# Performance work log

Hardware: AMD Instinct MI355X
Metric: run time of the kernel (lower is better)

## Reference

```python
import jax, jax.numpy as jnp
import numpy as np


def setup_inputs() -> dict:
    key = jax.random.key(0)
    k1, k2, k3 = jax.random.split(key, 3)
    shape = (2, 16, 2048, 64)  # (b, num_heads, seq_len, d_k)
    Q = jax.random.normal(k1, shape, dtype=jnp.float32)
    K = jax.random.normal(k2, shape, dtype=jnp.float32)
    V = jax.random.normal(k3, shape, dtype=jnp.float32)
    return {"Q": Q, "K": K, "V": V}


def reference(Q, K, V):
    # Mathematically identical to the blockwise online-softmax loop:
    # causal softmax attention with scale 1/sqrt(d_k), plus logsumexp L.
    d_k = Q.shape[-1]
    seq_len = Q.shape[2]
    scale = 1.0 / np.sqrt(d_k).astype(np.float32)
    # scores: [b, h, q, k]
    S = jnp.einsum("bhqd,bhkd->bhqk", Q, K) * scale
    causal_mask = jnp.tril(jnp.ones((seq_len, seq_len), dtype=bool))  # k_pos <= q_pos
    S = jnp.where(causal_mask, S, -jnp.inf)
    # L_i = m_i + log(l_i) == logsumexp over key dim (every row has >=1 valid key)
    L = jax.nn.logsumexp(S, axis=-1, keepdims=True)  # [b, h, q, 1]
    P = jnp.exp(S - L)  # normalized probabilities (deferred-normalization result)
    O = jnp.einsum("bhqk,bhkd->bhqd", P, V)
    return O, L
```

## Files before the change

### kernel.cpp

```cpp
#include <hip/hip_runtime.h>
#include <hip/hip_bf16.h>

#define S_LEN 2048
#define DH    64
#define NBH   32
#define KSCALE 0.1803368801111f
#define LN2    0.6931471805599453f
#define MB2    4.0f

typedef short v4s __attribute__((ext_vector_type(4)));
typedef short v8s __attribute__((ext_vector_type(8)));
typedef float v4f __attribute__((ext_vector_type(4)));

__device__ __forceinline__ unsigned short f2bf(float f){
  union { float f; unsigned int u; } v; v.f = f;
  return (unsigned short)((v.u + 0x7FFFu + ((v.u >> 16) & 1u)) >> 16);
}

__device__ __forceinline__ void gld16(void* lds, const void* g){
  __builtin_amdgcn_global_load_lds(
      (const __attribute__((address_space(1))) unsigned int*)g,
      (__attribute__((address_space(3))) unsigned int*)lds, 16, 0, 0);
}

__global__ __launch_bounds__(256) void prep(const float* __restrict__ K,
                                            const float* __restrict__ V,
                                            unsigned short* __restrict__ Kf,
                                            unsigned short* __restrict__ Vf){
  __shared__ unsigned short s[64 * 72];
  const int t   = blockIdx.x;
  const int bh  = blockIdx.y;
  const int tid = threadIdx.x;

  const float* Ksrc = K + ((size_t)bh * S_LEN + t * 64) * DH;
  #pragma unroll
  for (int i = 0; i < 4; ++i){
    int f = tid + i * 256;
    float4 v = ((const float4*)Ksrc)[f];
    int row = f >> 4, col = (f & 15) * 4;
    ushort4 o; o.x = f2bf(v.x); o.y = f2bf(v.y); o.z = f2bf(v.z); o.w = f2bf(v.w);
    *(ushort4*)(&s[row * 72 + col]) = o;
  }
  __syncthreads();
  unsigned short* KfT = Kf + ((size_t)bh * 32 + t) * 4096;
  #pragma unroll
  for (int i = 0; i < 2; ++i){
    int item = tid + i * 256;
    int c = item >> 6, l = item & 63;
    int kb = c >> 1, h = c & 1;
    v8s frag = *(const v8s*)(&s[(kb * 16 + (l & 15)) * 72 + h * 32 + (l >> 4) * 8]);
    *(v8s*)(&KfT[c * 512 + l * 8]) = frag;
  }
  __syncthreads();

  const float* Vsrc = V + ((size_t)bh * S_LEN + t * 64) * DH;
  #pragma unroll
  for (int i = 0; i < 4; ++i){
    int f = tid + i * 256;
    float4 v = ((const float4*)Vsrc)[f];
    int k = f >> 4, d = (f & 15) * 4;
    s[(d + 0) * 72 + k] = f2bf(v.x);
    s[(d + 1) * 72 + k] = f2bf(v.y);
    s[(d + 2) * 72 + k] = f2bf(v.z);
    s[(d + 3) * 72 + k] = f2bf(v.w);
  }
  __syncthreads();
  unsigned short* VfT = Vf + ((size_t)bh * 32 + t) * 4096;
  #pragma unroll
  for (int i = 0; i < 2; ++i){
    int item = tid + i * 256;
    int c = item >> 6, l = item & 63;
    int kb = c >> 1, dp = c & 1;
    int kk = kb * 16 + (l >> 4) * 4;
    v4s a = *(const v4s*)(&s[((dp * 2 + 0) * 16 + (l & 15)) * 72 + kk]);
    v4s b = *(const v4s*)(&s[((dp * 2 + 1) * 16 + (l & 15)) * 72 + kk]);
    v8s fr; fr[0]=a[0]; fr[1]=a[1]; fr[2]=a[2]; fr[3]=a[3];
            fr[4]=b[0]; fr[5]=b[1]; fr[6]=b[2]; fr[7]=b[3];
    *(v8s*)(&VfT[c * 512 + l * 8]) = fr;
  }
}

__global__ __launch_bounds__(256, 3) void fa_fwd(
    const float* __restrict__ Q,
    const unsigned short* __restrict__ Kf,
    const unsigned short* __restrict__ Vf,
    float* __restrict__ O, float* __restrict__ L)
{
  __shared__ __align__(16) char smem[2][16384];

  const int tid  = threadIdx.x;
  const int w    = tid >> 6;
  const int lane = tid & 63;
  const int lq   = lane & 15;
  const int g    = lane >> 4;
  const int bid  = blockIdx.x;
  const int o    = bid >> 5;
  const int hi   = o >> 3, lo = o & 7;
  const int qt   = hi * 8 + ((hi & 1) ? (7 - lo) : lo);
  const int bh   = bid & 31;
  const int M    = qt + 1;

  const unsigned short* KfB = Kf + (size_t)bh * 32 * 4096;
  const unsigned short* VfB = Vf + (size_t)bh * 32 * 4096;

  auto issue = [&](int t, char* buf){
    #pragma unroll
    for (int i = 0; i < 2; ++i){
      const int slot = tid + i * 256;
      gld16(buf        + slot * 16, KfB + (size_t)t * 4096 + slot * 8);
      gld16(buf + 8192 + slot * 16, VfB + (size_t)t * 4096 + slot * 8);
    }
  };

  v8s qf[4][2];
  #pragma unroll
  for (int s = 0; s < 4; ++s){
    const float* qp = Q + (size_t)(bh * S_LEN + qt * 64 + s * 16 + lq) * DH + g * 8;
    #pragma unroll
    for (int h = 0; h < 2; ++h){
      float4 a = *(const float4*)(qp + h * 32);
      float4 b = *(const float4*)(qp + h * 32 + 4);
      v8s qv;
      qv[0]=(short)f2bf(a.x*KSCALE); qv[1]=(short)f2bf(a.y*KSCALE);
      qv[2]=(short)f2bf(a.z*KSCALE); qv[3]=(short)f2bf(a.w*KSCALE);
      qv[4]=(short)f2bf(b.x*KSCALE); qv[5]=(short)f2bf(b.y*KSCALE);
      qv[6]=(short)f2bf(b.z*KSCALE); qv[7]=(short)f2bf(b.w*KSCALE);
      qf[s][h] = qv;
    }
  }

  issue(0, smem[0]);

  const v4f zero  = {0.f, 0.f, 0.f, 0.f};
  const v4f minit = {-MB2, -MB2, -MB2, -MB2};
  v4f acc[4][4];
  #pragma unroll
  for (int s = 0; s < 4; ++s)
    #pragma unroll
    for (int db = 0; db < 4; ++db) acc[s][db] = zero;
  float l4[4] = {0.f, 0.f, 0.f, 0.f};

  const int kb    = w;
  const int koff0 = (kb * 2    ) * 1024 + lane * 16;
  const int koff1 = (kb * 2 + 1) * 1024 + lane * 16;

  for (int t = 0; t < M; ++t){
    const int tn = (t + 1 < M) ? t + 1 : t;
    issue(tn, smem[(t + 1) & 1]);
    asm volatile("s_waitcnt vmcnt(4)" ::: "memory");
    __builtin_amdgcn_s_barrier();
    __builtin_amdgcn_sched_barrier(0);

    const char* kbase = smem[t & 1];
    const char* vbase = smem[t & 1] + 8192;

    v8s kf0 = *(const v8s*)(kbase + koff0);
    v8s kf1 = *(const v8s*)(kbase + koff1);
    v8s vv0 = *(const v8s*)(vbase + koff0);
    v8s vv1 = *(const v8s*)(vbase + koff1);
    v4s vv[4] = { {vv0[0],vv0[1],vv0[2],vv0[3]}, {vv0[4],vv0[5],vv0[6],vv0[7]},
                  {vv1[0],vv1[1],vv1[2],vv1[3]}, {vv1[4],vv1[5],vv1[6],vv1[7]} };

    float p4[4][4];
    __builtin_amdgcn_s_setprio(1);
    #pragma unroll
    for (int s = 0; s < 4; ++s){
      v4f st = minit;
      st = __builtin_amdgcn_mfma_f32_16x16x32_bf16(kf0, qf[s][0], st, 0, 0, 0);
      st = __builtin_amdgcn_mfma_f32_16x16x32_bf16(kf1, qf[s][1], st, 0, 0, 0);
      p4[s][0] = st[0]; p4[s][1] = st[1]; p4[s][2] = st[2]; p4[s][3] = st[3];
    }
    __builtin_amdgcn_s_setprio(0);

    if (t == qt){
      #pragma unroll
      for (int s = 0; s < 4; ++s)
        #pragma unroll
        for (int r = 0; r < 4; ++r)
          if (kb * 16 + g * 4 + r > s * 16 + lq) p4[s][r] = -INFINITY;
    }

    v4s pf[4];
    #pragma unroll
    for (int s = 0; s < 4; ++s){
      #pragma unroll
      for (int r = 0; r < 4; ++r){
        const float pe = __builtin_amdgcn_exp2f(p4[s][r]);
        p4[s][r] = pe;
        l4[s] += pe;
      }
      unsigned u0, u1;
      asm("v_cvt_pk_bf16_f32 %0, %1, %2" : "=v"(u0) : "v"(p4[s][0]), "v"(p4[s][1]));
      asm("v_cvt_pk_bf16_f32 %0, %1, %2" : "=v"(u1) : "v"(p4[s][2]), "v"(p4[s][3]));
      union { unsigned u[2]; v4s s4; } P; P.u[0] = u0; P.u[1] = u1;
      pf[s] = P.s4;
    }

    __builtin_amdgcn_s_setprio(1);
    #pragma unroll
    for (int s = 0; s < 4; ++s){
      acc[s][0] = __builtin_amdgcn_mfma_f32_16x16x16bf16_1k(vv[0], pf[s], acc[s][0], 0, 0, 0);
      acc[s][1] = __builtin_amdgcn_mfma_f32_16x16x16bf16_1k(vv[1], pf[s], acc[s][1], 0, 0, 0);
      acc[s][2] = __builtin_amdgcn_mfma_f32_16x16x16bf16_1k(vv[2], pf[s], acc[s][2], 0, 0, 0);
      acc[s][3] = __builtin_amdgcn_mfma_f32_16x16x16bf16_1k(vv[3], pf[s], acc[s][3], 0, 0, 0);
    }
    __builtin_amdgcn_s_setprio(0);
    __builtin_amdgcn_s_barrier();
    __builtin_amdgcn_sched_barrier(0);
  }

  asm volatile("s_waitcnt vmcnt(0)" ::: "memory");
  __builtin_amdgcn_sched_barrier(0);
  __syncthreads();

  #pragma unroll
  for (int s = 0; s < 4; ++s){
    l4[s] += __shfl_xor(l4[s], 16);
    l4[s] += __shfl_xor(l4[s], 32);
  }
  float* Lr = (float*)smem[1];
  if (lane < 16){
    #pragma unroll
    for (int s = 0; s < 4; ++s) Lr[(w * 4 + s) * 16 + lane] = l4[s];
  }
  __syncthreads();
  const float lfw = Lr[(0 * 4 + w) * 16 + lq] + Lr[(1 * 4 + w) * 16 + lq]
                  + Lr[(2 * 4 + w) * 16 + lq] + Lr[(3 * 4 + w) * 16 + lq];
  const float invw = 1.f / lfw;

  v4f* Or = (v4f*)smem[0];
  float* Ob = O + ((size_t)bh * S_LEN + qt * 64 + w * 16 + lq) * DH;
  #pragma unroll
  for (int db = 0; db < 4; ++db){
    __syncthreads();
    #pragma unroll
    for (int s = 0; s < 4; ++s) Or[((w * 4 + s) * 16 + lq) * 4 + g] = acc[s][db];
    __syncthreads();
    v4f o2 = Or[((0 * 4 + w) * 16 + lq) * 4 + g] + Or[((1 * 4 + w) * 16 + lq) * 4 + g]
           + Or[((2 * 4 + w) * 16 + lq) * 4 + g] + Or[((3 * 4 + w) * 16 + lq) * 4 + g];
    o2 *= invw;
    *(v4f*)(Ob + db * 16 + g * 4) = o2;
  }
  if (lane < 16)
    L[(size_t)bh * S_LEN + qt * 64 + w * 16 + lane] = logf(lfw) + MB2 * LN2;
}

__global__ __launch_bounds__(64) void fa_naive(
    const float* __restrict__ Q, const float* __restrict__ K,
    const float* __restrict__ V, float* __restrict__ O, float* __restrict__ L)
{
  const int q  = blockIdx.x;
  const int bh = blockIdx.y;
  const int d  = threadIdx.x;
  const float qv = Q[(size_t)(bh * S_LEN + q) * DH + d];
  float m = -INFINITY, l = 0.f, o = 0.f;
  for (int k = 0; k <= q; ++k){
    float s = qv * K[(size_t)(bh * S_LEN + k) * DH + d];
    #pragma unroll
    for (int off = 32; off > 0; off >>= 1) s += __shfl_xor(s, off);
    s *= 0.125f;
    const float mn = fmaxf(m, s);
    const float sfc = expf(m - mn);
    const float pe = expf(s - mn);
    l = l * sfc + pe;
    o = o * sfc + pe * V[(size_t)(bh * S_LEN + k) * DH + d];
    m = mn;
  }
  O[(size_t)(bh * S_LEN + q) * DH + d] = o / l;
  if (d == 0) L[(size_t)bh * S_LEN + q] = m + logf(l);
}

extern "C" void kernel_launch(void* const* d_in, const int* in_sizes, int n_in,
                              void* d_out, int out_size, void* d_ws, size_t ws_size,
                              hipStream_t stream)
{
  (void)in_sizes; (void)n_in; (void)out_size;
  const float* Q = (const float*)d_in[0];
  const float* K = (const float*)d_in[1];
  const float* V = (const float*)d_in[2];
  float* O = (float*)d_out;
  float* L = O + (size_t)NBH * S_LEN * DH;

  const size_t half = (size_t)NBH * S_LEN * DH * sizeof(unsigned short);
  if (ws_size >= 2 * half){
    unsigned short* Kf = (unsigned short*)d_ws;
    unsigned short* Vf = Kf + (size_t)NBH * S_LEN * DH;
    prep<<<dim3(S_LEN / 64, NBH), 256, 0, stream>>>(K, V, Kf, Vf);
    fa_fwd<<<dim3(1024), 256, 0, stream>>>(Q, Kf, Vf, O, L);
  } else {
    fa_naive<<<dim3(S_LEN, NBH), 64, 0, stream>>>(Q, K, V, O, L);
  }
}
```

Before: 47.50 us.

## Split work over 8 waves by query subtile and key half, skip dead diagonal

Moves the attention kernel from 4 waves per block, each owning one 16-key slice across all 64 queries, to 8 waves, each owning one 16-query subtile and one 32-key half. This cuts per-wave accumulator registers, which allows higher occupancy (launch bounds 512,8) and a simpler two-way final reduction. Waves whose key half lies entirely above the diagonal skip the masked diagonal tile. The cost is more waves contending at each barrier, and K and V fragments are now read from LDS inside the loop.

```diff
diff --git a/kernel.cpp b/kernel.cpp
--- a/kernel.cpp
+++ b/kernel.cpp
@@ -80,7 +80,7 @@
   }
 }
 
-__global__ __launch_bounds__(256, 3) void fa_fwd(
+__global__ __launch_bounds__(512, 8) void fa_fwd(
     const float* __restrict__ Q,
     const unsigned short* __restrict__ Kf,
     const unsigned short* __restrict__ Vf,
@@ -93,6 +93,8 @@
   const int lane = tid & 63;
   const int lq   = lane & 15;
   const int g    = lane >> 4;
+  const int kq   = w >> 2;
+  const int qs   = w & 3;
   const int bid  = blockIdx.x;
   const int o    = bid >> 5;
   const int hi   = o >> 3, lo = o & 7;
@@ -104,18 +106,13 @@
   const unsigned short* VfB = Vf + (size_t)bh * 32 * 4096;
 
   auto issue = [&](int t, char* buf){
-    #pragma unroll
-    for (int i = 0; i < 2; ++i){
-      const int slot = tid + i * 256;
-      gld16(buf        + slot * 16, KfB + (size_t)t * 4096 + slot * 8);
-      gld16(buf + 8192 + slot * 16, VfB + (size_t)t * 4096 + slot * 8);
-    }
+    gld16(buf +        tid * 16, KfB + (size_t)t * 4096 + tid * 8);
+    gld16(buf + 8192 + tid * 16, VfB + (size_t)t * 4096 + tid * 8);
   };
 
-  v8s qf[4][2];
-  #pragma unroll
-  for (int s = 0; s < 4; ++s){
-    const float* qp = Q + (size_t)(bh * S_LEN + qt * 64 + s * 16 + lq) * DH + g * 8;
+  v8s qf[2];
+  {
+    const float* qp = Q + (size_t)(bh * S_LEN + qt * 64 + qs * 16 + lq) * DH + g * 8;
     #pragma unroll
     for (int h = 0; h < 2; ++h){
       float4 a = *(const float4*)(qp + h * 32);
@@ -125,7 +122,7 @@
       qv[2]=(short)f2bf(a.z*KSCALE); qv[3]=(short)f2bf(a.w*KSCALE);
       qv[4]=(short)f2bf(b.x*KSCALE); qv[5]=(short)f2bf(b.y*KSCALE);
       qv[6]=(short)f2bf(b.z*KSCALE); qv[7]=(short)f2bf(b.w*KSCALE);
-      qf[s][h] = qv;
+      qf[h] = qv;
     }
   }
 
@@ -133,78 +130,77 @@
 
   const v4f zero  = {0.f, 0.f, 0.f, 0.f};
   const v4f minit = {-MB2, -MB2, -MB2, -MB2};
-  v4f acc[4][4];
-  #pragma unroll
-  for (int s = 0; s < 4; ++s)
-    #pragma unroll
-    for (int db = 0; db < 4; ++db) acc[s][db] = zero;
-  float l4[4] = {0.f, 0.f, 0.f, 0.f};
-
-  const int kb    = w;
-  const int koff0 = (kb * 2    ) * 1024 + lane * 16;
-  const int koff1 = (kb * 2 + 1) * 1024 + lane * 16;
+  v4f acc[4];
+  acc[0] = zero; acc[1] = zero; acc[2] = zero; acc[3] = zero;
+  float l1 = 0.f;
+
+  const int kb0 = kq * 2, kb1 = kq * 2 + 1;
+  const bool diagLive = (kq * 32 <= qs * 16 + 15);
 
   for (int t = 0; t < M; ++t){
     const int tn = (t + 1 < M) ? t + 1 : t;
     issue(tn, smem[(t + 1) & 1]);
-    asm volatile("s_waitcnt vmcnt(4)" ::: "memory");
+    asm volatile("s_waitcnt vmcnt(2)" ::: "memory");
     __builtin_amdgcn_s_barrier();
     __builtin_amdgcn_sched_barrier(0);
 
-    const char* kbase = smem[t & 1];
-    const char* vbase = smem[t & 1] + 8192;
-
-    v8s kf0 = *(const v8s*)(kbase + koff0);
-    v8s kf1 = *(const v8s*)(kbase + koff1);
-    v8s vv0 = *(const v8s*)(vbase + koff0);
-    v8s vv1 = *(const v8s*)(vbase + koff1);
-    v4s vv[4] = { {vv0[0],vv0[1],vv0[2],vv0[3]}, {vv0[4],vv0[5],vv0[6],vv0[7]},
-                  {vv1[0],vv1[1],vv1[2],vv1[3]}, {vv1[4],vv1[5],vv1[6],vv1[7]} };
-
-    float p4[4][4];
-    __builtin_amdgcn_s_setprio(1);
-    #pragma unroll
-    for (int s = 0; s < 4; ++s){
-      v4f st = minit;
-      st = __builtin_amdgcn_mfma_f32_16x16x32_bf16(kf0, qf[s][0], st, 0, 0, 0);
-      st = __builtin_amdgcn_mfma_f32_16x16x32_bf16(kf1, qf[s][1], st, 0, 0, 0);
-      p4[s][0] = st[0]; p4[s][1] = st[1]; p4[s][2] = st[2]; p4[s][3] = st[3];
+    if (t < qt || diagLive){
+      const char* kbase = smem[t & 1];
+      const char* vbase = smem[t & 1] + 8192;
+
+      float p4[2][4];
+      __builtin_amdgcn_s_setprio(1);
+      #pragma unroll
+      for (int j = 0; j < 2; ++j){
+        const int kb = kq * 2 + j;
+        v8s kf0 = *(const v8s*)(kbase + (kb * 2    ) * 1024 + lane * 16);
+        v8s kf1 = *(const v8s*)(kbase + (kb * 2 + 1) * 1024 + lane * 16);
+        v4f st = minit;
+        st = __builtin_amdgcn_mfma_f32_16x16x32_bf16(kf0, qf[0], st, 0, 0, 0);
+        st = __builtin_amdgcn_mfma_f32_16x16x32_bf16(kf1, qf[1], st, 0, 0, 0);
+        p4[j][0] = st[0]; p4[j][1] = st[1]; p4[j][2] = st[2]; p4[j][3] = st[3];
+      }
+      __builtin_amdgcn_s_setprio(0);
+
+      if (t == qt){
+        #pragma unroll
+        for (int j = 0; j < 2; ++j)
+          #pragma unroll
+          for (int r = 0; r < 4; ++r)
+            if (kq * 32 + j * 16 + g * 4 + r > qs * 16 + lq) p4[j][r] = -INFINITY;
+      }
+
+      v4s pf[2];
+      #pragma unroll
+      for (int j = 0; j < 2; ++j){
+        #pragma unroll
+        for (int r = 0; r < 4; ++r){
+          const float pe = __builtin_amdgcn_exp2f(p4[j][r]);
+          p4[j][r] = pe;
+          l1 += pe;
+        }
+        unsigned u0, u1;
+        asm("v_cvt_pk_bf16_f32 %0, %1, %2" : "=v"(u0) : "v"(p4[j][0]), "v"(p4[j][1]));
+        asm("v_cvt_pk_bf16_f32 %0, %1, %2" : "=v"(u1) : "v"(p4[j][2]), "v"(p4[j][3]));
+        union { unsigned u[2]; v4s s4; } P; P.u[0] = u0; P.u[1] = u1;
+        pf[j] = P.s4;
+      }
+
+      __builtin_amdgcn_s_setprio(1);
+      #pragma unroll
+      for (int j = 0; j < 2; ++j){
+        const int kb = kq * 2 + j;
+        #pragma unroll
+        for (int dp = 0; dp < 2; ++dp){
+          v8s vv8 = *(const v8s*)(vbase + (kb * 2 + dp) * 1024 + lane * 16);
+          v4s va0 = {vv8[0], vv8[1], vv8[2], vv8[3]};
+          v4s va1 = {vv8[4], vv8[5], vv8[6], vv8[7]};
+          acc[dp * 2    ] = __builtin_amdgcn_mfma_f32_16x16x16bf16_1k(va0, pf[j], acc[dp * 2    ], 0, 0, 0);
+          acc[dp * 2 + 1] = __builtin_amdgcn_mfma_f32_16x16x16bf16_1k(va1, pf[j], acc[dp * 2 + 1], 0, 0, 0);
+        }
+      }
+      __builtin_amdgcn_s_setprio(0);
     }
-    __builtin_amdgcn_s_setprio(0);
-
-    if (t == qt){
-      #pragma unroll
-      for (int s = 0; s < 4; ++s)
-        #pragma unroll
-        for (int r = 0; r < 4; ++r)
-          if (kb * 16 + g * 4 + r > s * 16 + lq) p4[s][r] = -INFINITY;
-    }
-
-    v4s pf[4];
-    #pragma unroll
-    for (int s = 0; s < 4; ++s){
-      #pragma unroll
-      for (int r = 0; r < 4; ++r){
-        const float pe = __builtin_amdgcn_exp2f(p4[s][r]);
-        p4[s][r] = pe;
-        l4[s] += pe;
-      }
-      unsigned u0, u1;
-      asm("v_cvt_pk_bf16_f32 %0, %1, %2" : "=v"(u0) : "v"(p4[s][0]), "v"(p4[s][1]));
-      asm("v_cvt_pk_bf16_f32 %0, %1, %2" : "=v"(u1) : "v"(p4[s][2]), "v"(p4[s][3]));
-      union { unsigned u[2]; v4s s4; } P; P.u[0] = u0; P.u[1] = u1;
-      pf[s] = P.s4;
-    }
-
-    __builtin_amdgcn_s_setprio(1);
-    #pragma unroll
-    for (int s = 0; s < 4; ++s){
-      acc[s][0] = __builtin_amdgcn_mfma_f32_16x16x16bf16_1k(vv[0], pf[s], acc[s][0], 0, 0, 0);
-      acc[s][1] = __builtin_amdgcn_mfma_f32_16x16x16bf16_1k(vv[1], pf[s], acc[s][1], 0, 0, 0);
-      acc[s][2] = __builtin_amdgcn_mfma_f32_16x16x16bf16_1k(vv[2], pf[s], acc[s][2], 0, 0, 0);
-      acc[s][3] = __builtin_amdgcn_mfma_f32_16x16x16bf16_1k(vv[3], pf[s], acc[s][3], 0, 0, 0);
-    }
-    __builtin_amdgcn_s_setprio(0);
     __builtin_amdgcn_s_barrier();
     __builtin_amdgcn_sched_barrier(0);
   }
@@ -213,36 +209,30 @@
   __builtin_amdgcn_sched_barrier(0);
   __syncthreads();
 
-  #pragma unroll
-  for (int s = 0; s < 4; ++s){
-    l4[s] += __shfl_xor(l4[s], 16);
-    l4[s] += __shfl_xor(l4[s], 32);
-  }
-  float* Lr = (float*)smem[1];
-  if (lane < 16){
-    #pragma unroll
-    for (int s = 0; s < 4; ++s) Lr[(w * 4 + s) * 16 + lane] = l4[s];
-  }
-  __syncthreads();
-  const float lfw = Lr[(0 * 4 + w) * 16 + lq] + Lr[(1 * 4 + w) * 16 + lq]
-                  + Lr[(2 * 4 + w) * 16 + lq] + Lr[(3 * 4 + w) * 16 + lq];
-  const float invw = 1.f / lfw;
-
-  v4f* Or = (v4f*)smem[0];
-  float* Ob = O + ((size_t)bh * S_LEN + qt * 64 + w * 16 + lq) * DH;
-  #pragma unroll
-  for (int db = 0; db < 4; ++db){
-    __syncthreads();
-    #pragma unroll
-    for (int s = 0; s < 4; ++s) Or[((w * 4 + s) * 16 + lq) * 4 + g] = acc[s][db];
-    __syncthreads();
-    v4f o2 = Or[((0 * 4 + w) * 16 + lq) * 4 + g] + Or[((1 * 4 + w) * 16 + lq) * 4 + g]
-           + Or[((2 * 4 + w) * 16 + lq) * 4 + g] + Or[((3 * 4 + w) * 16 + lq) * 4 + g];
-    o2 *= invw;
-    *(v4f*)(Ob + db * 16 + g * 4) = o2;
-  }
-  if (lane < 16)
-    L[(size_t)bh * S_LEN + qt * 64 + w * 16 + lane] = logf(lfw) + MB2 * LN2;
+  l1 += __shfl_xor(l1, 16);
+  l1 += __shfl_xor(l1, 32);
+
+  float* Lx = (float*)(smem[1]);
+  v4f*  Ox = (v4f*)(smem[0]);
+  if (kq == 1){
+    if (lane < 16) Lx[qs * 16 + lane] = l1;
+    #pragma unroll
+    for (int db = 0; db < 4; ++db)
+      Ox[(qs * 4 + db) * 64 + lane] = acc[db];
+  }
+  __syncthreads();
+  if (kq == 0){
+    const float lt   = l1 + Lx[qs * 16 + lq];
+    const float invl = 1.f / lt;
+    float* Ob = O + ((size_t)bh * S_LEN + qt * 64 + qs * 16 + lq) * DH;
+    #pragma unroll
+    for (int db = 0; db < 4; ++db){
+      v4f o2 = (acc[db] + Ox[(qs * 4 + db) * 64 + lane]) * invl;
+      *(v4f*)(Ob + db * 16 + g * 4) = o2;
+    }
+    if (lane < 16)
+      L[(size_t)bh * S_LEN + qt * 64 + qs * 16 + lane] = logf(lt) + MB2 * LN2;
+  }
 }
 
 __global__ __launch_bounds__(64) void fa_naive(
@@ -286,7 +276,7 @@
     unsigned short* Kf = (unsigned short*)d_ws;
     unsigned short* Vf = Kf + (size_t)NBH * S_LEN * DH;
     prep<<<dim3(S_LEN / 64, NBH), 256, 0, stream>>>(K, V, Kf, Vf);
-    fa_fwd<<<dim3(1024), 256, 0, stream>>>(Q, Kf, Vf, O, L);
+    fa_fwd<<<dim3(1024), 512, 0, stream>>>(Q, Kf, Vf, O, L);
   } else {
     fa_naive<<<dim3(S_LEN, NBH), 64, 0, stream>>>(Q, K, V, O, L);
   }
```

Measured after the change: 43.82 us. -7.8%, faster.
